# Kernel optimization log

Hardware: AMD Instinct MI355X
Metric: run time of the kernel (lower is better)

## Reference

```python
import jax, jax.numpy as jnp
import numpy as np

N_NODES = 100000
N_EDGES = 3200000


def setup_inputs() -> dict:
    key = jax.random.key(0)
    ks = jax.random.split(key, 8)
    x = jax.random.normal(ks[0], (N_NODES, 128), dtype=jnp.float32)
    edge_index = jax.random.randint(ks[1], (2, N_EDGES), 0, N_NODES, dtype=jnp.int64)
    edge_weight = jax.random.uniform(ks[2], (N_EDGES,), dtype=jnp.float32)
    W1 = jax.random.normal(ks[3], (128, 32), dtype=jnp.float32) * (1.0 / np.sqrt(128))
    b1 = jnp.zeros((32,), dtype=jnp.float32)
    W2 = jax.random.normal(ks[4], (32, 16), dtype=jnp.float32) * (1.0 / np.sqrt(32))
    b2 = jnp.zeros((16,), dtype=jnp.float32)
    Wfc = jax.random.normal(ks[5], (16, 1), dtype=jnp.float32) * (1.0 / np.sqrt(16))
    bfc = jnp.zeros((1,), dtype=jnp.float32)
    return {"x": x, "edge_index": edge_index, "edge_weight": edge_weight,
            "W1": W1, "b1": b1, "W2": W2, "b2": b2, "Wfc": Wfc, "bfc": bfc}


def _gcn_norm(edge_index, edge_weight, num_nodes):
    # PyG gcn_norm: add self-loops (weight 1), sym-normalize by in-degree of target (col)
    row, col = edge_index[0], edge_index[1]
    loop = jnp.arange(num_nodes, dtype=row.dtype)
    row_f = jnp.concatenate([row, loop])
    col_f = jnp.concatenate([col, loop])
    w_f = jnp.concatenate([edge_weight, jnp.ones((num_nodes,), edge_weight.dtype)])
    deg = jax.ops.segment_sum(w_f, col_f, num_segments=num_nodes)
    dinv = jnp.where(deg > 0, deg ** -0.5, 0.0)
    norm_w = dinv[row_f] * w_f * dinv[col_f]  # [E+N]
    return row_f, col_f, norm_w


def _gcn_conv(x, row_f, col_f, norm_w, W, b, num_nodes):
    h = x @ W                      # transform first (in->out dims)
    msg = h[row_f] * norm_w[:, None]  # gather source features, scale by edge norm
    out = jax.ops.segment_sum(msg, col_f, num_segments=num_nodes)  # scatter-add to targets
    return out + b


def reference(x, edge_index, edge_weight, W1, b1, W2, b2, Wfc, bfc):
    N = x.shape[0]
    row_f, col_f, norm_w = _gcn_norm(edge_index, edge_weight, N)
    h = jax.nn.leaky_relu(_gcn_conv(x, row_f, col_f, norm_w, W1, b1, N))
    # dropout is identity in eval mode; norm=False skips GraphNorm
    h = jax.nn.leaky_relu(_gcn_conv(h, row_f, col_f, norm_w, W2, b2, N))
    return h @ Wfc + bfc  # [N, 1]
```

## Files before the change

### kernel.cpp

```cpp
#include <hip/hip_runtime.h>
#include <hip/hip_fp16.h>

#define N_NODES 100000
#define N_EDGES 3200000
#define BSHIFT 8
#define BSIZE 256
#define NB ((N_NODES + BSIZE - 1) / BSIZE)
#define ROWBITS 17
#define ROWMASK ((1 << ROWBITS) - 1)
#define EB_GRID ((N_EDGES + 4095) / 4096)


__global__ void k_detect(const unsigned* __restrict__ w, int* __restrict__ flag) {
    __shared__ unsigned s[256];
    unsigned v = 0;
    for (int t = threadIdx.x; t < 4096; t += 256) v |= w[2 * t + 1];
    s[threadIdx.x] = v;
    __syncthreads();
    for (int off = 128; off > 0; off >>= 1) {
        if (threadIdx.x < (unsigned)off) s[threadIdx.x] |= s[threadIdx.x + off];
        __syncthreads();
    }
    if (threadIdx.x == 0) flag[0] = (s[0] == 0) ? 1 : 0;
}

__device__ __forceinline__ void load_edge(const unsigned* __restrict__ e, int f, int E,
                                          int i, int& r, int& c) {
    if (f) { r = (int)e[2 * i]; c = (int)e[2 * E + 2 * i]; }
    else   { r = (int)e[i];     c = (int)e[E + i]; }
}


__global__ __launch_bounds__(256) void k_bcnt(const unsigned* __restrict__ eidx,
                                              const int* __restrict__ flag,
                                              int* __restrict__ bcnt, int E, int n) {
    __shared__ int lc[NB];
    for (int i = threadIdx.x; i < NB; i += 256) lc[i] = 0;
    __syncthreads();
    int f = flag[0];
    int base = blockIdx.x * 4096;
    for (int i = 0; i < 16; ++i) {
        int e = base + i * 256 + threadIdx.x;
        if (e < E) {
            int r, c;
            load_edge(eidx, f, E, e, r, c);
            if ((unsigned)r < (unsigned)n && (unsigned)c < (unsigned)n)
                atomicAdd(&lc[c >> BSHIFT], 1);
        }
    }
    __syncthreads();
    for (int i = threadIdx.x; i < NB; i += 256)
        if (lc[i]) atomicAdd(&bcnt[i], lc[i]);
}

__global__ __launch_bounds__(512) void k_bscan(const int* __restrict__ bcnt,
                                               int* __restrict__ bbase,
                                               int* __restrict__ gcursor,
                                               int* __restrict__ start) {
    __shared__ int s[512];
    int tid = threadIdx.x;
    int v = (tid < NB) ? bcnt[tid] : 0;
    s[tid] = v;
    __syncthreads();
    for (int o = 1; o < 512; o <<= 1) {
        int t = (tid >= o) ? s[tid - o] : 0;
        __syncthreads();
        s[tid] += t;
        __syncthreads();
    }
    if (tid < NB) {
        int excl = s[tid] - v;
        bbase[tid] = excl;
        gcursor[tid] = excl;
    }
    if (tid == 511) {
        bbase[NB] = s[511];
        start[N_NODES] = s[511];
    }
}

__global__ __launch_bounds__(256) void k_bucket(const unsigned* __restrict__ eidx,
                                                const int* __restrict__ flag,
                                                const float* __restrict__ ew,
                                                int* __restrict__ gcursor,
                                                int2* __restrict__ bstage, int E, int n) {
    __shared__ int lcnt[NB];
    __shared__ int lbase[NB];
    __shared__ int lcur[NB];
    int tid = threadIdx.x;
    for (int i = tid; i < NB; i += 256) { lcnt[i] = 0; lcur[i] = 0; }
    __syncthreads();
    int f = flag[0];
    int base = blockIdx.x * 4096;
    int rr[16], cc[16];
    float wwv[16];
#pragma unroll
    for (int i = 0; i < 16; ++i) {
        int e = base + i * 256 + tid;
        rr[i] = -1; cc[i] = 0; wwv[i] = 0.f;
        if (e < E) {
            int r, c;
            load_edge(eidx, f, E, e, r, c);
            if ((unsigned)r < (unsigned)n && (unsigned)c < (unsigned)n) {
                rr[i] = r; cc[i] = c; wwv[i] = ew[e];
            }
        }
    }
#pragma unroll
    for (int i = 0; i < 16; ++i)
        if (rr[i] >= 0) atomicAdd(&lcnt[cc[i] >> BSHIFT], 1);
    __syncthreads();
    for (int i = tid; i < NB; i += 256)
        lbase[i] = atomicAdd(&gcursor[i], lcnt[i]);
    __syncthreads();
#pragma unroll
    for (int i = 0; i < 16; ++i) {
        if (rr[i] >= 0) {
            int b = cc[i] >> BSHIFT, off = cc[i] & (BSIZE - 1);
            int p = lbase[b] + atomicAdd(&lcur[b], 1);
            bstage[p] = make_int2((off << ROWBITS) | rr[i], __float_as_int(wwv[i]));
        }
    }
}

__global__ __launch_bounds__(256) void k_passb(const int2* __restrict__ bstage,
                                               const int* __restrict__ bbase,
                                               int* __restrict__ start,
                                               float* __restrict__ dinv,
                                               int2* __restrict__ erw, int n) {
    __shared__ int   cnt[BSIZE];
    __shared__ float wsm[BSIZE];
    __shared__ int   cur[BSIZE];
    int tid = threadIdx.x;
    int b = blockIdx.x;
    int n0 = b << BSHIFT;
    int nn = min(BSIZE, n - n0);
    int bb = bbase[b], be = bbase[b + 1];
    cnt[tid] = 0;
    wsm[tid] = 0.f;
    __syncthreads();
    for (int e = bb + tid; e < be; e += 256) {
        int2 kv = bstage[e];
        int off = kv.x >> ROWBITS;
        atomicAdd(&cnt[off], 1);
        atomicAdd(&wsm[off], __int_as_float(kv.y));
    }
    __syncthreads();
    int v = cnt[tid];
    for (int o = 1; o < 256; o <<= 1) {
        int t = (tid >= o) ? cnt[tid - o] : 0;
        __syncthreads();
        cnt[tid] += t;
        __syncthreads();
    }
    int excl = cnt[tid] - v;
    if (tid < nn) {
        start[n0 + tid] = bb + excl;
        dinv[n0 + tid] = 1.0f / sqrtf(1.0f + wsm[tid]);
    }
    cur[tid] = excl;
    __syncthreads();
    for (int e = bb + tid; e < be; e += 256) {
        int2 kv = bstage[e];
        int off = kv.x >> ROWBITS;
        int p = bb + atomicAdd(&cur[off], 1);
        erw[p] = make_int2(kv.x & ROWMASK, kv.y);
    }
}


__global__ __launch_bounds__(256) void k_gemm1(const float* __restrict__ x,
                                               const float* __restrict__ W1,
                                               const float* __restrict__ dinv,
                                               __half* __restrict__ g1, int n) {
    __shared__ float W1s[128 * 32];
    __shared__ float xs[8][128];
    int tid = threadIdx.x;
    for (int i = tid; i < 128 * 32; i += 256) W1s[i] = W1[i];
    int node0 = blockIdx.x * 8;
    for (int i = tid; i < 8 * 128; i += 256) {
        int ln = i >> 7, ii = i & 127;
        int node = node0 + ln;
        xs[ln][ii] = (node < n) ? x[node * 128 + ii] : 0.f;
    }
    __syncthreads();
    int ln = tid >> 5;
    int kk = tid & 31;
    int node = node0 + ln;
    if (node < n) {
        float acc = 0.f;
#pragma unroll
        for (int i = 0; i < 128; ++i) acc += xs[ln][i] * W1s[i * 32 + kk];
        g1[node * 32 + kk] = __float2half(dinv[node] * acc);
    }
}


__global__ __launch_bounds__(256) void k_agg1(const __half* __restrict__ g,
                                              const int* __restrict__ start,
                                              const int2* __restrict__ erw,
                                              const float* __restrict__ dinv,
                                              const float* __restrict__ b1,
                                              float* __restrict__ h, int n) {
    int wid = (blockIdx.x * 256 + threadIdx.x) >> 6;
    int l = threadIdx.x & 63;
    if (wid >= n) return;
    int slot = l >> 3;
    int cg   = l & 7;
    int s = start[wid], en = start[wid + 1];
    float4 acc = make_float4(0.f, 0.f, 0.f, 0.f);
    for (int e0 = s; e0 < en; e0 += 8) {
        int e = e0 + slot;
        if (e < en) {
            int2 rw = erw[e];
            float w = __int_as_float(rw.y);
            float2 raw = *reinterpret_cast<const float2*>(g + ((size_t)rw.x << 5) + (cg << 2));
            __half2 h01 = *reinterpret_cast<const __half2*>(&raw.x);
            __half2 h23 = *reinterpret_cast<const __half2*>(&raw.y);
            float2 f01 = __half22float2(h01), f23 = __half22float2(h23);
            acc.x += w * f01.x; acc.y += w * f01.y;
            acc.z += w * f23.x; acc.w += w * f23.y;
        }
    }
#pragma unroll
    for (int m = 8; m <= 32; m <<= 1) {
        acc.x += __shfl_xor(acc.x, m);
        acc.y += __shfl_xor(acc.y, m);
        acc.z += __shfl_xor(acc.z, m);
        acc.w += __shfl_xor(acc.w, m);
    }
    if (slot == 0) {
        float2 raw = *reinterpret_cast<const float2*>(g + ((size_t)wid << 5) + (cg << 2));
        __half2 h01 = *reinterpret_cast<const __half2*>(&raw.x);
        __half2 h23 = *reinterpret_cast<const __half2*>(&raw.y);
        float2 f01 = __half22float2(h01), f23 = __half22float2(h23);
        float di = dinv[wid];
        float4 b = *reinterpret_cast<const float4*>(b1 + (cg << 2));
        float4 v;
        v.x = di * (acc.x + f01.x) + b.x;
        v.y = di * (acc.y + f01.y) + b.y;
        v.z = di * (acc.z + f23.x) + b.z;
        v.w = di * (acc.w + f23.y) + b.w;
        v.x = v.x > 0.f ? v.x : 0.01f * v.x;
        v.y = v.y > 0.f ? v.y : 0.01f * v.y;
        v.z = v.z > 0.f ? v.z : 0.01f * v.z;
        v.w = v.w > 0.f ? v.w : 0.01f * v.w;
        *reinterpret_cast<float4*>(h + ((size_t)wid << 5) + (cg << 2)) = v;
    }
}


__global__ __launch_bounds__(256) void k_gemm2(const float* __restrict__ h1,
                                               const float* __restrict__ W2,
                                               const float* __restrict__ dinv,
                                               __half* __restrict__ g2, int n) {
    __shared__ float W2s[32 * 16];
    int tid = threadIdx.x;
    for (int i = tid; i < 32 * 16; i += 256) W2s[i] = W2[i];
    __syncthreads();
    int t = blockIdx.x * 256 + tid;
    if (t < n * 16) {
        int node = t >> 4, j = t & 15;
        float acc = 0.f;
#pragma unroll
        for (int k = 0; k < 32; ++k) acc += h1[node * 32 + k] * W2s[k * 16 + j];
        g2[t] = __float2half(dinv[node] * acc);
    }
}


__global__ __launch_bounds__(256) void k_agg2(const __half* __restrict__ g2,
                                              const int* __restrict__ start,
                                              const int2* __restrict__ erw,
                                              const float* __restrict__ dinv,
                                              const float* __restrict__ b2,
                                              const float* __restrict__ Wfc,
                                              const float* __restrict__ bfc,
                                              float* __restrict__ out, int n) {
    int wid = (blockIdx.x * 256 + threadIdx.x) >> 6;
    int l = threadIdx.x & 63;
    if (wid >= n) return;
    int slot = l >> 2;
    int cg   = l & 3;
    int s = start[wid], en = start[wid + 1];
    float4 acc = make_float4(0.f, 0.f, 0.f, 0.f);
    for (int e0 = s; e0 < en; e0 += 16) {
        int e = e0 + slot;
        if (e < en) {
            int2 rw = erw[e];
            float w = __int_as_float(rw.y);
            float2 raw = *reinterpret_cast<const float2*>(g2 + ((size_t)rw.x << 4) + (cg << 2));
            __half2 h01 = *reinterpret_cast<const __half2*>(&raw.x);
            __half2 h23 = *reinterpret_cast<const __half2*>(&raw.y);
            float2 f01 = __half22float2(h01), f23 = __half22float2(h23);
            acc.x += w * f01.x; acc.y += w * f01.y;
            acc.z += w * f23.x; acc.w += w * f23.y;
        }
    }
#pragma unroll
    for (int m = 4; m <= 32; m <<= 1) {
        acc.x += __shfl_xor(acc.x, m);
        acc.y += __shfl_xor(acc.y, m);
        acc.z += __shfl_xor(acc.z, m);
        acc.w += __shfl_xor(acc.w, m);
    }
    float2 raw = *reinterpret_cast<const float2*>(g2 + ((size_t)wid << 4) + (cg << 2));
    __half2 h01 = *reinterpret_cast<const __half2*>(&raw.x);
    __half2 h23 = *reinterpret_cast<const __half2*>(&raw.y);
    float2 f01 = __half22float2(h01), f23 = __half22float2(h23);
    float di = dinv[wid];
    float4 b = *reinterpret_cast<const float4*>(b2 + (cg << 2));
    float4 wf = *reinterpret_cast<const float4*>(Wfc + (cg << 2));
    float4 v;
    v.x = di * (acc.x + f01.x) + b.x;
    v.y = di * (acc.y + f01.y) + b.y;
    v.z = di * (acc.z + f23.x) + b.z;
    v.w = di * (acc.w + f23.y) + b.w;
    v.x = v.x > 0.f ? v.x : 0.01f * v.x;
    v.y = v.y > 0.f ? v.y : 0.01f * v.y;
    v.z = v.z > 0.f ? v.z : 0.01f * v.z;
    v.w = v.w > 0.f ? v.w : 0.01f * v.w;
    float p = v.x * wf.x + v.y * wf.y + v.z * wf.z + v.w * wf.w;
    p += __shfl_xor(p, 1);
    p += __shfl_xor(p, 2);
    if (l == 0) out[wid] = p + bfc[0];
}

extern "C" void kernel_launch(void* const* d_in, const int* in_sizes, int n_in,
                              void* d_out, int out_size, void* d_ws, size_t ws_size,
                              hipStream_t stream) {
    const float*    x    = (const float*)d_in[0];
    const unsigned* eidx = (const unsigned*)d_in[1];
    const float*    ew   = (const float*)d_in[2];
    const float*    W1   = (const float*)d_in[3];
    const float*    b1   = (const float*)d_in[4];
    const float*    W2   = (const float*)d_in[5];
    const float*    b2   = (const float*)d_in[6];
    const float*    Wfc  = (const float*)d_in[7];
    const float*    bfc  = (const float*)d_in[8];
    float* out = (float*)d_out;

    const int N = N_NODES;
    const int E = N_EDGES;

    char* ws = (char*)d_ws;
    int*    flag    = (int*)ws;
    int*    bcnt    = (int*)(ws + 4096);
    int*    bbase   = (int*)(ws + 8192);
    int*    gcursor = (int*)(ws + 16384);
    int*    start   = (int*)(ws + 65536);
    float*  dinv    = (float*)(ws + 512u * 1024);
    int2*   erw     = (int2*)(ws + 1u  * 1024 * 1024);
    int2*   bstage  = (int2*)(ws + 27u * 1024 * 1024);
    __half* g1h     = (__half*)(ws + 27u * 1024 * 1024);
    float*  h1      = (float*)(ws + 34u * 1024 * 1024);
    __half* g2h     = (__half*)(ws + 47u * 1024 * 1024);

    k_detect<<<1, 256, 0, stream>>>(eidx, flag);

    hipMemsetAsync(bcnt, 0, (size_t)NB * sizeof(int), stream);
    k_bcnt<<<EB_GRID, 256, 0, stream>>>(eidx, flag, bcnt, E, N);
    k_bscan<<<1, 512, 0, stream>>>(bcnt, bbase, gcursor, start);
    k_bucket<<<EB_GRID, 256, 0, stream>>>(eidx, flag, ew, gcursor, bstage, E, N);
    k_passb<<<NB, 256, 0, stream>>>(bstage, bbase, start, dinv, erw, N);

    k_gemm1<<<(N + 7) / 8, 256, 0, stream>>>(x, W1, dinv, g1h, N);
    {
        int blocks = (int)(((long long)N * 64 + 255) / 256);
        k_agg1<<<blocks, 256, 0, stream>>>(g1h, start, erw, dinv, b1, h1, N);
    }

    k_gemm2<<<(N * 16 + 255) / 256, 256, 0, stream>>>(h1, W2, dinv, g2h, N);
    {
        int blocks = (int)(((long long)N * 64 + 255) / 256);
        k_agg2<<<blocks, 256, 0, stream>>>(g2h, start, erw, dinv, b2, Wfc, bfc, out, N);
    }
}
```

Before: 426.2 us.

## Replace count-scan-bucket CSR build with fixed-capacity buckets and LDS staging

```diff
diff --git a/kernel.cpp b/kernel.cpp
--- a/kernel.cpp
+++ b/kernel.cpp
@@ -3,12 +3,13 @@
 
 #define N_NODES 100000
 #define N_EDGES 3200000
-#define BSHIFT 8
-#define BSIZE 256
+#define BSHIFT 7
+#define BSIZE 128
 #define NB ((N_NODES + BSIZE - 1) / BSIZE)
+#define CAP 4736
 #define ROWBITS 17
 #define ROWMASK ((1 << ROWBITS) - 1)
-#define EB_GRID ((N_EDGES + 4095) / 4096)
+#define EB2 ((N_EDGES + 2047) / 2048)
 
 
 __global__ void k_detect(const unsigned* __restrict__ w, int* __restrict__ flag) {
@@ -31,59 +32,11 @@
 }
 
 
-__global__ __launch_bounds__(256) void k_bcnt(const unsigned* __restrict__ eidx,
-                                              const int* __restrict__ flag,
-                                              int* __restrict__ bcnt, int E, int n) {
-    __shared__ int lc[NB];
-    for (int i = threadIdx.x; i < NB; i += 256) lc[i] = 0;
-    __syncthreads();
-    int f = flag[0];
-    int base = blockIdx.x * 4096;
-    for (int i = 0; i < 16; ++i) {
-        int e = base + i * 256 + threadIdx.x;
-        if (e < E) {
-            int r, c;
-            load_edge(eidx, f, E, e, r, c);
-            if ((unsigned)r < (unsigned)n && (unsigned)c < (unsigned)n)
-                atomicAdd(&lc[c >> BSHIFT], 1);
-        }
-    }
-    __syncthreads();
-    for (int i = threadIdx.x; i < NB; i += 256)
-        if (lc[i]) atomicAdd(&bcnt[i], lc[i]);
-}
-
-__global__ __launch_bounds__(512) void k_bscan(const int* __restrict__ bcnt,
-                                               int* __restrict__ bbase,
-                                               int* __restrict__ gcursor,
-                                               int* __restrict__ start) {
-    __shared__ int s[512];
-    int tid = threadIdx.x;
-    int v = (tid < NB) ? bcnt[tid] : 0;
-    s[tid] = v;
-    __syncthreads();
-    for (int o = 1; o < 512; o <<= 1) {
-        int t = (tid >= o) ? s[tid - o] : 0;
-        __syncthreads();
-        s[tid] += t;
-        __syncthreads();
-    }
-    if (tid < NB) {
-        int excl = s[tid] - v;
-        bbase[tid] = excl;
-        gcursor[tid] = excl;
-    }
-    if (tid == 511) {
-        bbase[NB] = s[511];
-        start[N_NODES] = s[511];
-    }
-}
-
-__global__ __launch_bounds__(256) void k_bucket(const unsigned* __restrict__ eidx,
-                                                const int* __restrict__ flag,
-                                                const float* __restrict__ ew,
-                                                int* __restrict__ gcursor,
-                                                int2* __restrict__ bstage, int E, int n) {
+__global__ __launch_bounds__(256) void k_scatter(const unsigned* __restrict__ eidx,
+                                                 const int* __restrict__ flag,
+                                                 const float* __restrict__ ew,
+                                                 int* __restrict__ gcursor,
+                                                 int2* __restrict__ bstage, int E, int n) {
     __shared__ int lcnt[NB];
     __shared__ int lbase[NB];
     __shared__ int lcur[NB];
@@ -91,56 +44,62 @@
     for (int i = tid; i < NB; i += 256) { lcnt[i] = 0; lcur[i] = 0; }
     __syncthreads();
     int f = flag[0];
-    int base = blockIdx.x * 4096;
-    int rr[16], cc[16];
-    float wwv[16];
-#pragma unroll
-    for (int i = 0; i < 16; ++i) {
+    int base = blockIdx.x * 2048;
+    int rr[8], cc[8];
+    float wv[8];
+#pragma unroll
+    for (int i = 0; i < 8; ++i) {
         int e = base + i * 256 + tid;
-        rr[i] = -1; cc[i] = 0; wwv[i] = 0.f;
+        rr[i] = -1; cc[i] = 0; wv[i] = 0.f;
         if (e < E) {
             int r, c;
             load_edge(eidx, f, E, e, r, c);
             if ((unsigned)r < (unsigned)n && (unsigned)c < (unsigned)n) {
-                rr[i] = r; cc[i] = c; wwv[i] = ew[e];
+                rr[i] = r; cc[i] = c; wv[i] = ew[e];
             }
         }
     }
 #pragma unroll
-    for (int i = 0; i < 16; ++i)
+    for (int i = 0; i < 8; ++i)
         if (rr[i] >= 0) atomicAdd(&lcnt[cc[i] >> BSHIFT], 1);
     __syncthreads();
     for (int i = tid; i < NB; i += 256)
-        lbase[i] = atomicAdd(&gcursor[i], lcnt[i]);
-    __syncthreads();
-#pragma unroll
-    for (int i = 0; i < 16; ++i) {
+        if (lcnt[i]) lbase[i] = atomicAdd(&gcursor[i], lcnt[i]);
+    __syncthreads();
+#pragma unroll
+    for (int i = 0; i < 8; ++i) {
         if (rr[i] >= 0) {
             int b = cc[i] >> BSHIFT, off = cc[i] & (BSIZE - 1);
-            int p = lbase[b] + atomicAdd(&lcur[b], 1);
-            bstage[p] = make_int2((off << ROWBITS) | rr[i], __float_as_int(wwv[i]));
+            int pos = lbase[b] + atomicAdd(&lcur[b], 1);
+            if (pos < CAP)
+                bstage[(size_t)b * CAP + pos] =
+                    make_int2((off << ROWBITS) | rr[i], __float_as_int(wv[i]));
         }
     }
 }
 
-__global__ __launch_bounds__(256) void k_passb(const int2* __restrict__ bstage,
-                                               const int* __restrict__ bbase,
+
+__global__ __launch_bounds__(256) void k_passb(const int* __restrict__ gcursor,
+                                               int2* __restrict__ erw,
                                                int* __restrict__ start,
-                                               float* __restrict__ dinv,
-                                               int2* __restrict__ erw, int n) {
-    __shared__ int   cnt[BSIZE];
+                                               int* __restrict__ end,
+                                               float* __restrict__ dinv, int n) {
+    __shared__ int2  se[CAP];
+    __shared__ int   cnt[256];
     __shared__ float wsm[BSIZE];
     __shared__ int   cur[BSIZE];
     int tid = threadIdx.x;
     int b = blockIdx.x;
     int n0 = b << BSHIFT;
     int nn = min(BSIZE, n - n0);
-    int bb = bbase[b], be = bbase[b + 1];
+    size_t bb = (size_t)b * CAP;
+    int cntE = min(gcursor[b], CAP);
     cnt[tid] = 0;
-    wsm[tid] = 0.f;
-    __syncthreads();
-    for (int e = bb + tid; e < be; e += 256) {
-        int2 kv = bstage[e];
+    if (tid < BSIZE) wsm[tid] = 0.f;
+    __syncthreads();
+    for (int e = tid; e < cntE; e += 256) {
+        int2 kv = erw[bb + e];
+        se[e] = kv;
         int off = kv.x >> ROWBITS;
         atomicAdd(&cnt[off], 1);
         atomicAdd(&wsm[off], __int_as_float(kv.y));
@@ -155,16 +114,17 @@
     }
     int excl = cnt[tid] - v;
     if (tid < nn) {
-        start[n0 + tid] = bb + excl;
-        dinv[n0 + tid] = 1.0f / sqrtf(1.0f + wsm[tid]);
-    }
-    cur[tid] = excl;
-    __syncthreads();
-    for (int e = bb + tid; e < be; e += 256) {
-        int2 kv = bstage[e];
+        start[n0 + tid] = (int)bb + excl;
+        end[n0 + tid]   = (int)bb + excl + v;
+        dinv[n0 + tid]  = 1.0f / sqrtf(1.0f + wsm[tid]);
+    }
+    if (tid < BSIZE) cur[tid] = excl;
+    __syncthreads();
+    for (int e = tid; e < cntE; e += 256) {
+        int2 kv = se[e];
         int off = kv.x >> ROWBITS;
-        int p = bb + atomicAdd(&cur[off], 1);
-        erw[p] = make_int2(kv.x & ROWMASK, kv.y);
+        int p = atomicAdd(&cur[off], 1);
+        erw[bb + p] = make_int2(kv.x & ROWMASK, kv.y);
     }
 }
 
@@ -176,12 +136,15 @@
     __shared__ float W1s[128 * 32];
     __shared__ float xs[8][128];
     int tid = threadIdx.x;
-    for (int i = tid; i < 128 * 32; i += 256) W1s[i] = W1[i];
+    for (int i = tid; i < 1024; i += 256)
+        *reinterpret_cast<float4*>(W1s + 4 * i) = reinterpret_cast<const float4*>(W1)[i];
     int node0 = blockIdx.x * 8;
-    for (int i = tid; i < 8 * 128; i += 256) {
-        int ln = i >> 7, ii = i & 127;
+    {
+        int ln = tid >> 5, ii = tid & 31;
         int node = node0 + ln;
-        xs[ln][ii] = (node < n) ? x[node * 128 + ii] : 0.f;
+        float4 vv = make_float4(0.f, 0.f, 0.f, 0.f);
+        if (node < n) vv = reinterpret_cast<const float4*>(x)[node * 32 + ii];
+        *reinterpret_cast<float4*>(&xs[ln][4 * ii]) = vv;
     }
     __syncthreads();
     int ln = tid >> 5;
@@ -198,6 +161,7 @@
 
 __global__ __launch_bounds__(256) void k_agg1(const __half* __restrict__ g,
                                               const int* __restrict__ start,
+                                              const int* __restrict__ end,
                                               const int2* __restrict__ erw,
                                               const float* __restrict__ dinv,
                                               const float* __restrict__ b1,
@@ -207,7 +171,7 @@
     if (wid >= n) return;
     int slot = l >> 3;
     int cg   = l & 7;
-    int s = start[wid], en = start[wid + 1];
+    int s = start[wid], en = end[wid];
     float4 acc = make_float4(0.f, 0.f, 0.f, 0.f);
     for (int e0 = s; e0 < en; e0 += 8) {
         int e = e0 + slot;
@@ -271,6 +235,7 @@
 
 __global__ __launch_bounds__(256) void k_agg2(const __half* __restrict__ g2,
                                               const int* __restrict__ start,
+                                              const int* __restrict__ end,
                                               const int2* __restrict__ erw,
                                               const float* __restrict__ dinv,
                                               const float* __restrict__ b2,
@@ -282,7 +247,7 @@
     if (wid >= n) return;
     int slot = l >> 2;
     int cg   = l & 3;
-    int s = start[wid], en = start[wid + 1];
+    int s = start[wid], en = end[wid];
     float4 acc = make_float4(0.f, 0.f, 0.f, 0.f);
     for (int e0 = s; e0 < en; e0 += 16) {
         int e = e0 + slot;
@@ -345,34 +310,30 @@
 
     char* ws = (char*)d_ws;
     int*    flag    = (int*)ws;
-    int*    bcnt    = (int*)(ws + 4096);
-    int*    bbase   = (int*)(ws + 8192);
-    int*    gcursor = (int*)(ws + 16384);
-    int*    start   = (int*)(ws + 65536);
-    float*  dinv    = (float*)(ws + 512u * 1024);
-    int2*   erw     = (int2*)(ws + 1u  * 1024 * 1024);
-    int2*   bstage  = (int2*)(ws + 27u * 1024 * 1024);
-    __half* g1h     = (__half*)(ws + 27u * 1024 * 1024);
-    float*  h1      = (float*)(ws + 34u * 1024 * 1024);
-    __half* g2h     = (__half*)(ws + 47u * 1024 * 1024);
+    int*    gcursor = (int*)(ws + 4096);
+    int*    start   = (int*)(ws + 64u * 1024);
+    int*    end     = (int*)(ws + 512u * 1024);
+    float*  dinv    = (float*)(ws + 1024u * 1024);
+    int2*   erw     = (int2*)(ws + 2u * 1024 * 1024);
+    __half* g1h     = (__half*)(ws + 32u * 1024 * 1024);
+    float*  h1      = (float*)(ws + 39u * 1024 * 1024);
+    __half* g2h     = (__half*)(ws + 52u * 1024 * 1024);
 
     k_detect<<<1, 256, 0, stream>>>(eidx, flag);
 
-    hipMemsetAsync(bcnt, 0, (size_t)NB * sizeof(int), stream);
-    k_bcnt<<<EB_GRID, 256, 0, stream>>>(eidx, flag, bcnt, E, N);
-    k_bscan<<<1, 512, 0, stream>>>(bcnt, bbase, gcursor, start);
-    k_bucket<<<EB_GRID, 256, 0, stream>>>(eidx, flag, ew, gcursor, bstage, E, N);
-    k_passb<<<NB, 256, 0, stream>>>(bstage, bbase, start, dinv, erw, N);
+    hipMemsetAsync(gcursor, 0, (size_t)NB * sizeof(int), stream);
+    k_scatter<<<EB2, 256, 0, stream>>>(eidx, flag, ew, gcursor, erw, E, N);
+    k_passb<<<NB, 256, 0, stream>>>(gcursor, erw, start, end, dinv, N);
 
     k_gemm1<<<(N + 7) / 8, 256, 0, stream>>>(x, W1, dinv, g1h, N);
     {
         int blocks = (int)(((long long)N * 64 + 255) / 256);
-        k_agg1<<<blocks, 256, 0, stream>>>(g1h, start, erw, dinv, b1, h1, N);
+        k_agg1<<<blocks, 256, 0, stream>>>(g1h, start, end, erw, dinv, b1, h1, N);
     }
 
     k_gemm2<<<(N * 16 + 255) / 256, 256, 0, stream>>>(h1, W2, dinv, g2h, N);
     {
         int blocks = (int)(((long long)N * 64 + 255) / 256);
-        k_agg2<<<blocks, 256, 0, stream>>>(g2h, start, erw, dinv, b2, Wfc, bfc, out, N);
-    }
-}
+        k_agg2<<<blocks, 256, 0, stream>>>(g2h, start, end, erw, dinv, b2, Wfc, bfc, out, N);
+    }
+}
```

Measured after the change: 373.2 us. -12.4%, faster.
